# Kernel optimization log

Hardware: AMD Instinct MI355X
Metric: run time of the kernel (lower is better)

## Reference

```python
import jax, jax.numpy as jnp
import numpy as np

INPUT_DIM = 16
NUM_MFS = 4
NUM_RULES = 1024
NUM_CLASSES = 10
BATCH = 4096


def setup_inputs() -> dict:
    key = jax.random.key(0)
    k1, k2, k3, k4, k5 = jax.random.split(key, 5)
    x = jax.random.normal(k1, (BATCH, INPUT_DIM), dtype=jnp.float32)
    centers = jax.random.normal(k2, (INPUT_DIM, NUM_MFS), dtype=jnp.float32)
    # widths must be positive (used as std of gaussian)
    widths = jax.random.uniform(k3, (INPUT_DIM, NUM_MFS), dtype=jnp.float32, minval=0.2, maxval=1.2)
    consequents = jax.random.normal(k4, (NUM_RULES, INPUT_DIM + 1, NUM_CLASSES), dtype=jnp.float32)
    rule_idx = jax.random.randint(k5, (INPUT_DIM, NUM_RULES), 0, NUM_MFS, dtype=jnp.int32)
    return {"x": x, "centers": centers, "widths": widths,
            "consequents": consequents, "rule_idx": rule_idx}


def reference(x, centers, widths, consequents, rule_idx):
    B, D = x.shape
    # Gaussian membership functions: [B, D, M]
    mfs = jnp.exp(-((x[:, :, None] - centers[None]) ** 2) / (2.0 * widths[None] ** 2) + 1e-9)
    # Gather rule-specific memberships: [B, D, R]
    d_idx = jnp.arange(D)[:, None]  # [D, 1] broadcasts with rule_idx [D, R]
    rule_mfs = mfs[:, d_idx, rule_idx]
    # Firing strengths (product over input dims) and normalization: [B, R]
    firing = jnp.prod(rule_mfs, axis=1)
    norm_fs = firing / (jnp.sum(firing, axis=1, keepdims=True) + 1e-9)
    # Extended input with bias column: [B, D+1]
    x_ext = jnp.concatenate([x, jnp.ones((B, 1), dtype=x.dtype)], axis=1)
    # phi = norm_fs[:, :, None] * x_ext[:, None, :]; y = phi_flat @ beta_flat
    # expressed as a single contraction (same math, phi is detached w.r.t. x_ext)
    y_hat = jnp.einsum('br,bi,ric->bc', norm_fs, jax.lax.stop_gradient(x_ext), consequents)
    return y_hat, norm_fs, x_ext
```

## Files before the change

kernel.cpp:

```cpp
#include <hip/hip_runtime.h>

#define B 4096
#define D 16
#define R 1024
#define NC 10
#define IC 170
#define NT 11
#define NP 176
#define KSPLIT 4
#define RPB (R / KSPLIT)
#define BT 16
#define GSP 192
#define TSTR 72

typedef __attribute__((ext_vector_type(8))) short short8;
typedef __attribute__((ext_vector_type(4))) float f32x4;

__device__ __forceinline__ unsigned short f2bf(float f) {
    unsigned u = __float_as_uint(f);
    return (unsigned short)((u + 0x7fffu + ((u >> 16) & 1u)) >> 16);
}

__global__ __launch_bounds__(256) void prep_kernel(
    const float* __restrict__ cons, const int* __restrict__ rule_idx,
    const float* __restrict__ x, unsigned* __restrict__ packed,
    unsigned short* __restrict__ Bsw, float* __restrict__ out_y,
    float* __restrict__ out_xext)
{
    __shared__ unsigned short T[NP * TSTR];
    const int blk = blockIdx.x, tid = threadIdx.x;

    if (blk < 16) {
        const int k0 = blk * 64;
        for (int t = tid; t < 64 * IC; t += 256) {
            int k = t / IC, c = t - k * IC;
            T[c * TSTR + k] = f2bf(cons[(size_t)(k0 + k) * IC + c]);
        }
        for (int t = tid; t < (NP - IC) * 64; t += 256) {
            int c = IC + t / 64, k = t & 63;
            T[c * TSTR + k] = 0;
        }
        __syncthreads();
        for (int t = tid; t < NP * 8; t += 256) {
            int row = t >> 3, seg = t & 7;
            *(short8*)&Bsw[(size_t)row * R + k0 + seg * 8] =
                *(const short8*)&T[row * TSTR + seg * 8];
        }
    } else if (blk < 20) {
        int r = (blk - 16) * 256 + tid;
        unsigned bits = 0;
#pragma unroll
        for (int d = 0; d < D; ++d)
            bits |= (((unsigned)rule_idx[d * R + r]) & 3u) << (2 * d);
        packed[r] = bits;
    } else if (blk < 180) {
        out_y[(blk - 20) * 256 + tid] = 0.0f;
    } else {
        int t = (blk - 180) * 256 + tid;
        int b = t / 17, i = t - b * 17;
        out_xext[t] = (i < 16) ? x[b * D + i] : 1.0f;
    }
}

__global__ __launch_bounds__(256) void firing_kernel(
    const float* __restrict__ x, const float* __restrict__ centers,
    const float* __restrict__ widths, const unsigned* __restrict__ packed,
    float* __restrict__ out_norm)
{
    __shared__ float s_z[64];
    __shared__ float s_z2[8][16];
    __shared__ float s_z4[4 * 256];
    __shared__ float s_red[8];
    const int b = blockIdx.x, tid = threadIdx.x;

    if (tid < 64) {
        int d = tid >> 2;
        float xv = x[b * D + d];
        float c = centers[tid], w = widths[tid];
        float diff = xv - c;
        s_z[tid] = 1e-9f - diff * diff / (2.0f * w * w);
    }
    __syncthreads();
    if (tid < 128) {
        int p = tid >> 4, i = tid & 15;
        s_z2[p][i] = s_z[p * 8 + (i & 3)] + s_z[p * 8 + 4 + ((i >> 2) & 3)];
    }
    __syncthreads();
#pragma unroll
    for (int q = 0; q < 4; ++q)
        s_z4[q * 256 + tid] = s_z2[2 * q][tid & 15] + s_z2[2 * q + 1][(tid >> 4) & 15];
    __syncthreads();

    float f[4], lsum = 0.0f;
#pragma unroll
    for (int j = 0; j < 4; ++j) {
        unsigned w = packed[tid + 256 * j];
        float s = s_z4[w & 255] + s_z4[256 + ((w >> 8) & 255)]
                + s_z4[512 + ((w >> 16) & 255)] + s_z4[768 + (w >> 24)];
        f[j] = __expf(s);
        lsum += f[j];
    }
#pragma unroll
    for (int off = 1; off < 64; off <<= 1) lsum += __shfl_xor(lsum, off, 64);
    const int lane = tid & 63, wid = tid >> 6;
    if (lane == 0) s_red[wid] = lsum;
    __syncthreads();
    if (tid == 0) {
        float tot = s_red[0] + s_red[1] + s_red[2] + s_red[3] + 1e-9f;
        s_red[4] = 1.0f / tot;
    }
    __syncthreads();
    const float inv = s_red[4];
#pragma unroll
    for (int j = 0; j < 4; ++j)
        out_norm[(size_t)b * R + tid + 256 * j] = f[j] * inv;
}

__global__ __launch_bounds__(256, 4) void yhat_kernel(
    const float* __restrict__ norm, const unsigned short* __restrict__ Bsw,
    const float* __restrict__ x, float* __restrict__ out_y)
{
    __shared__ float Gs[BT * GSP];
    __shared__ float xe[BT * 17];

    const int tid = threadIdx.x;
    const int mt = blockIdx.x & 255;
    const int ks = blockIdx.x >> 8;
    const int bl0 = mt * BT;
    const int r_base = ks * RPB;

    for (int t = tid; t < BT * 17; t += 256) {
        int bl = t / 17, i = t - bl * 17;
        xe[t] = (i < 16) ? x[(size_t)(bl0 + bl) * D + i] : 1.0f;
    }

    const int lane = tid & 63, wv = tid >> 6;
    const int m_ = lane & 15, q_ = lane >> 4;
    const int nt0 = wv * 3;
    const int ntn = (wv == 3) ? 2 : 3;

    f32x4 acc[3];
    const f32x4 zf = {0.f, 0.f, 0.f, 0.f};
    acc[0] = zf; acc[1] = zf; acc[2] = zf;

    const float* aptr = &norm[(size_t)(bl0 + m_) * R + r_base + q_ * 8];
    const unsigned short* bptr = &Bsw[(size_t)r_base + q_ * 8];

#pragma unroll
    for (int kk = 0; kk < RPB; kk += 32) {
        float4 a0 = *(const float4*)(aptr + kk);
        float4 a1 = *(const float4*)(aptr + kk + 4);
        short8 a;
        a[0] = (short)f2bf(a0.x); a[1] = (short)f2bf(a0.y);
        a[2] = (short)f2bf(a0.z); a[3] = (short)f2bf(a0.w);
        a[4] = (short)f2bf(a1.x); a[5] = (short)f2bf(a1.y);
        a[6] = (short)f2bf(a1.z); a[7] = (short)f2bf(a1.w);
#pragma unroll
        for (int j = 0; j < 3; ++j) {
            if (j < ntn) {
                int row = (nt0 + j) * 16 + m_;
                short8 bf = *(const short8*)&bptr[(size_t)row * R + kk];
                acc[j] = __builtin_amdgcn_mfma_f32_16x16x32_bf16(a, bf, acc[j], 0, 0, 0);
            }
        }
    }

    __syncthreads();
#pragma unroll
    for (int j = 0; j < 3; ++j) {
        if (j < ntn) {
            int nt = nt0 + j;
#pragma unroll
            for (int r = 0; r < 4; ++r)
                Gs[(q_ * 4 + r) * GSP + nt * 16 + m_] = acc[j][r];
        }
    }
    __syncthreads();
    if (tid < BT * NC) {
        int bl = tid / NC, c = tid - bl * NC;
        float y = 0.0f;
#pragma unroll
        for (int i = 0; i < 17; ++i)
            y += xe[bl * 17 + i] * Gs[bl * GSP + i * NC + c];
        atomicAdd(&out_y[(size_t)(bl0 + bl) * NC + c], y);
    }
}

extern "C" void kernel_launch(void* const* d_in, const int* in_sizes, int n_in,
                              void* d_out, int out_size, void* d_ws, size_t ws_size,
                              hipStream_t stream) {
    const float* x        = (const float*)d_in[0];
    const float* centers  = (const float*)d_in[1];
    const float* widths   = (const float*)d_in[2];
    const float* cons     = (const float*)d_in[3];
    const int*   rule_idx = (const int*)d_in[4];

    float* out      = (float*)d_out;
    float* out_y    = out;
    float* out_norm = out + (size_t)B * NC;
    float* out_xext = out + (size_t)B * NC + (size_t)B * R;

    unsigned* packed     = (unsigned*)d_ws;
    unsigned short* Bsw  = (unsigned short*)((char*)d_ws + 4096);

    prep_kernel<<<452, 256, 0, stream>>>(cons, rule_idx, x, packed, Bsw, out_y, out_xext);
    firing_kernel<<<B, 256, 0, stream>>>(x, centers, widths, packed, out_norm);
    yhat_kernel<<<(B / BT) * KSPLIT, 256, 0, stream>>>(out_norm, Bsw, x, out_y);
}
```

Measured before the change: 102.3 us.

## Stage A and B tiles through shared memory in K chunks for yhat MFMA

```diff
diff --git a/kernel.cpp b/kernel.cpp
--- a/kernel.cpp
+++ b/kernel.cpp
@@ -7,9 +7,11 @@
 #define IC 170
 #define NT 11
 #define NP 176
+#define KC 64
 #define KSPLIT 4
 #define RPB (R / KSPLIT)
 #define BT 16
+#define BSTR 72
 #define GSP 192
 #define TSTR 72
 
@@ -120,7 +122,8 @@
     const float* __restrict__ norm, const unsigned short* __restrict__ Bsw,
     const float* __restrict__ x, float* __restrict__ out_y)
 {
-    __shared__ float Gs[BT * GSP];
+    __shared__ unsigned short Bs[NT * 16 * BSTR];
+    __shared__ unsigned short As[BT * BSTR];
     __shared__ float xe[BT * 17];
 
     const int tid = threadIdx.x;
@@ -143,29 +146,38 @@
     const f32x4 zf = {0.f, 0.f, 0.f, 0.f};
     acc[0] = zf; acc[1] = zf; acc[2] = zf;
 
-    const float* aptr = &norm[(size_t)(bl0 + m_) * R + r_base + q_ * 8];
-    const unsigned short* bptr = &Bsw[(size_t)r_base + q_ * 8];
-
-#pragma unroll
-    for (int kk = 0; kk < RPB; kk += 32) {
-        float4 a0 = *(const float4*)(aptr + kk);
-        float4 a1 = *(const float4*)(aptr + kk + 4);
-        short8 a;
-        a[0] = (short)f2bf(a0.x); a[1] = (short)f2bf(a0.y);
-        a[2] = (short)f2bf(a0.z); a[3] = (short)f2bf(a0.w);
-        a[4] = (short)f2bf(a1.x); a[5] = (short)f2bf(a1.y);
-        a[6] = (short)f2bf(a1.z); a[7] = (short)f2bf(a1.w);
-#pragma unroll
-        for (int j = 0; j < 3; ++j) {
-            if (j < ntn) {
-                int row = (nt0 + j) * 16 + m_;
-                short8 bf = *(const short8*)&bptr[(size_t)row * R + kk];
-                acc[j] = __builtin_amdgcn_mfma_f32_16x16x32_bf16(a, bf, acc[j], 0, 0, 0);
+    for (int c0 = 0; c0 < RPB; c0 += KC) {
+        const int kabs = r_base + c0;
+        __syncthreads();
+        for (int t = tid; t < NP * 8; t += 256) {
+            int row = t >> 3, seg = t & 7;
+            *(short8*)&Bs[row * BSTR + seg * 8] =
+                *(const short8*)&Bsw[row * R + kabs + seg * 8];
+        }
+        {
+            int row = tid >> 4, c4 = tid & 15;
+            float4 v = *(const float4*)&norm[(size_t)(bl0 + row) * R + kabs + c4 * 4];
+            ushort4 o;
+            o.x = f2bf(v.x); o.y = f2bf(v.y); o.z = f2bf(v.z); o.w = f2bf(v.w);
+            *(ushort4*)&As[row * BSTR + c4 * 4] = o;
+        }
+        __syncthreads();
+#pragma unroll
+        for (int kh = 0; kh < 2; ++kh) {
+            short8 a = *(const short8*)&As[m_ * BSTR + kh * 32 + q_ * 8];
+#pragma unroll
+            for (int j = 0; j < 3; ++j) {
+                if (j < ntn) {
+                    int nt = nt0 + j;
+                    short8 bfrag = *(const short8*)&Bs[(nt * 16 + m_) * BSTR + kh * 32 + q_ * 8];
+                    acc[j] = __builtin_amdgcn_mfma_f32_16x16x32_bf16(a, bfrag, acc[j], 0, 0, 0);
+                }
             }
         }
     }
 
     __syncthreads();
+    float* Gs = (float*)Bs;
 #pragma unroll
     for (int j = 0; j < 3; ++j) {
         if (j < ntn) {
```

New measurement: 96.62 us. 5.5% less time.
